# Optimization experiments

Measured on AMD Instinct MI355X. Metric: run time of the kernel, lower is better.

Reference implementation:

```python
import jax, jax.numpy as jnp
import numpy as np

PATCH = 16
CH = 3


def setup_inputs() -> dict:
    key = jax.random.key(0)
    k1, k2, k3 = jax.random.split(key, 3)
    B, H = 16, 512
    embed_dim = PATCH * PATCH * CH  # 768
    x = jax.random.normal(k1, (B, CH, H, H), dtype=jnp.float32)
    fan_in = CH * PATCH * PATCH
    w = jax.random.normal(k2, (embed_dim, CH, PATCH, PATCH), dtype=jnp.float32) / np.float32(np.sqrt(fan_in))
    b = jax.random.normal(k3, (embed_dim,), dtype=jnp.float32) * 0.01
    return {"x": x, "w": w, "b": b}


def reference(x, w, b):
    p = w.shape[2]                      # patch_size
    B, C, imgsize, _ = x.shape
    pn = imgsize // p                   # patch_num (NOTE: pre-padding count, as in source)
    # zero-pad by one patch on every side
    xp = jnp.pad(x, ((0, 0), (0, 0), (p, p), (p, p)))
    # strided patch-embed conv: [B, embed_dim, pn+2, pn+2]
    xt = jax.lax.conv_general_dilated(xp, w, window_strides=(p, p), padding='VALID')
    xt = xt + b[None, :, None, None]
    B1, C1, H1, W1 = xt.shape           # H1 = W1 = pn + 2
    xt = xt.reshape(B1, C1, H1 * W1)
    # same (buggy-looking but faithful) index set / stride-pn neighbors as the source
    idxs = jnp.array([i * pn + j for i in range(1, pn - 1) for j in range(1, pn)], dtype=jnp.int32)
    inv8 = jnp.float32(1.0 / 8.0)

    def body(buf, idx):
        # torch aliases x_final=x_temp, so reads see earlier in-place writes -> sequential scan
        s = (buf[:, :, idx - pn] + buf[:, :, idx + pn]
             + buf[:, :, idx - 1] + buf[:, :, idx + 1]
             + buf[:, :, idx - pn - 1] + buf[:, :, idx - pn + 1]
             + buf[:, :, idx + pn - 1] + buf[:, :, idx + pn + 1]) * inv8
        return buf.at[:, :, idx].set(s), None

    xf, _ = jax.lax.scan(body, xt, idxs)
    side = imgsize + 2 * p              # embed_dim*H1*W1 == C*side*side by construction
    out = xf.reshape(B1, C, side, side)
    return out[:, :, p:imgsize + p, p:imgsize + p]
```

## Files before the change

kernel.cpp:

```cpp
#include <hip/hip_runtime.h>
#include <hip/hip_bf16.h>


typedef __attribute__((ext_vector_type(8))) short s8v;
typedef __attribute__((ext_vector_type(4))) float f4v;
typedef __attribute__((ext_vector_type(8))) unsigned short us8;
typedef __attribute__((ext_vector_type(4))) unsigned short us4;

__device__ __forceinline__ unsigned short f2bf(float f) {
    __hip_bfloat16 h = __float2bfloat16(f);
    return *reinterpret_cast<unsigned short*>(&h);
}
__device__ __forceinline__ float bf2f(unsigned short u) {
    union { unsigned int i; float f; } c; c.i = (unsigned int)u << 16; return c.f;
}

__device__ __forceinline__ void gload_lds16(const void* g, void* l) {
    __builtin_amdgcn_global_load_lds(
        (const __attribute__((address_space(1))) unsigned int*)g,
        (__attribute__((address_space(3))) unsigned int*)l,
        16, 0, 0);
}

__global__ __launch_bounds__(256) void prep_k(const float* __restrict__ x,
                                              const float* __restrict__ w,
                                              unsigned short* __restrict__ a_bf,
                                              unsigned short* __restrict__ w_bf) {
    const int bid = blockIdx.x;
    if (bid < 6144) {
        int g = bid * 256 + threadIdx.x;
        int f = g << 3;
        int wc = f & 511;
        int h  = (f >> 9) & 511;
        int cb = f >> 18;
        int c  = cb % 3, b = cb / 3;
        const float4 v0 = *(const float4*)(x + f);
        const float4 v1 = *(const float4*)(x + f + 4);
        int m = (b << 10) + ((h >> 4) << 5) + (wc >> 4);
        int k = (c << 8) + ((h & 15) << 4) + (wc & 15);
        us8 o;
        o[0] = f2bf(v0.x); o[1] = f2bf(v0.y); o[2] = f2bf(v0.z); o[3] = f2bf(v0.w);
        o[4] = f2bf(v1.x); o[5] = f2bf(v1.y); o[6] = f2bf(v1.z); o[7] = f2bf(v1.w);
        *(us8*)(a_bf + (size_t)m * 768 + k) = o;
    } else {
        int g = (bid - 6144) * 256 + threadIdx.x;
        int f = g << 3;
        const float4 v0 = *(const float4*)(w + f);
        const float4 v1 = *(const float4*)(w + f + 4);
        us8 u;
        u[0] = f2bf(v0.x); u[1] = f2bf(v0.y); u[2] = f2bf(v0.z); u[3] = f2bf(v0.w);
        u[4] = f2bf(v1.x); u[5] = f2bf(v1.y); u[6] = f2bf(v1.z); u[7] = f2bf(v1.w);
        *(us8*)(w_bf + f) = u;
    }
}

__global__ __launch_bounds__(256) void conv_gemm_k(const unsigned short* __restrict__ A,
                                                   const unsigned short* __restrict__ W,
                                                   const float* __restrict__ bias,
                                                   unsigned short* __restrict__ xt) {
    __shared__ __align__(16) unsigned short As[2][128 * 32];
    __shared__ __align__(16) unsigned short Bs[2][128 * 32];
    const int tid  = threadIdx.x;
    const int lane = tid & 63, wv = tid >> 6;
    const int wr = wv >> 1, wc = wv & 1;
    const int m0 = blockIdx.x << 7, n0 = blockIdx.y << 7;
    const int bb = m0 >> 10;

    f4v acc[4][4] = {};

    const int l2 = lane >> 2;
    const int kx = ((lane & 3) ^ ((l2 >> 1) & 3)) << 3;
    const unsigned short* gA = A + (size_t)(m0 + (wv << 5) + l2) * 768 + kx;
    const unsigned short* gB = W + (size_t)(n0 + (wv << 5) + l2) * 768 + kx;

    auto stage = [&](int buf, int k0) {
        gload_lds16(gA + k0,            As[buf] + (wv << 10));
        gload_lds16(gA + k0 + 16 * 768, As[buf] + (wv << 10) + 512);
        gload_lds16(gB + k0,            Bs[buf] + (wv << 10));
        gload_lds16(gB + k0 + 16 * 768, Bs[buf] + (wv << 10) + 512);
    };

    stage(0, 0);
    asm volatile("s_waitcnt vmcnt(0)" ::: "memory");
    __syncthreads();

    const int cq = lane >> 4, l15 = lane & 15;
    int cur = 0;
    for (int t = 0; t < 24; ++t) {
        if (t < 23) stage(cur ^ 1, (t + 1) << 5);
        s8v a[4], b[4];
        #pragma unroll
        for (int mi = 0; mi < 4; ++mi) {
            int ra = (wr << 6) + (mi << 4) + l15;
            a[mi] = *(const s8v*)(As[cur] + (ra << 5) + ((cq ^ ((ra >> 1) & 3)) << 3));
        }
        #pragma unroll
        for (int ni = 0; ni < 4; ++ni) {
            int rb = (wc << 6) + (ni << 4) + l15;
            b[ni] = *(const s8v*)(Bs[cur] + (rb << 5) + ((cq ^ ((rb >> 1) & 3)) << 3));
        }
        #pragma unroll
        for (int mi = 0; mi < 4; ++mi)
            #pragma unroll
            for (int ni = 0; ni < 4; ++ni)
                acc[mi][ni] = __builtin_amdgcn_mfma_f32_16x16x32_bf16(a[mi], b[ni], acc[mi][ni], 0, 0, 0);
        asm volatile("s_waitcnt vmcnt(0)" ::: "memory");
        __syncthreads();
        cur ^= 1;
    }

    #pragma unroll
    for (int mi = 0; mi < 4; ++mi) {
        int m  = m0 + (wr << 6) + (mi << 4) + (cq << 2);
        int ph = (m >> 5) & 31, pwm = m & 31;
        unsigned short* dst = xt + (((size_t)bb * 768) << 10) + (ph << 5) + pwm;
        #pragma unroll
        for (int ni = 0; ni < 4; ++ni) {
            int n = n0 + (wc << 6) + (ni << 4) + l15;
            float bv = bias[n];
            us4 o;
            o[0] = f2bf(acc[mi][ni][0] + bv);
            o[1] = f2bf(acc[mi][ni][1] + bv);
            o[2] = f2bf(acc[mi][ni][2] + bv);
            o[3] = f2bf(acc[mi][ni][3] + bv);
            *(us4*)(dst + ((size_t)n << 10)) = o;
        }
    }
}

__global__ __launch_bounds__(256) void scan_emit_k(const unsigned short* __restrict__ xt,
                                                   const float* __restrict__ bias,
                                                   float* __restrict__ out) {
    const int grp = (blockIdx.x * 256 + threadIdx.x) >> 5;
    const int j   = threadIdx.x & 31;
    const int b   = grp / 768;
    const int c1  = grp - b * 768;
    const unsigned short* basep = xt + ((size_t)grp << 10);
    const float bias_c = bias[c1];
    float* baseo = out + (size_t)b * 786432 + (size_t)(c1 >> 8) * 262144;

    int rem = (c1 & 255) * 1156 + j;
    int ey  = rem / 544;
    int ex  = rem - ey * 544;
    int eo  = (ey - 16) * 512 + (ex - 16);

    auto estep = [&](float v) {
        if (((unsigned)(ex - 16) < 512u) & ((unsigned)(ey - 16) < 512u))
            baseo[eo] = v;
        ex += 32;
        int wrp = (ex >= 544);
        ex -= wrp ? 544 : 0;
        ey += wrp;
        eo += wrp ? 0 : 32;
    };
    auto sel = [&](int p) -> float {
        unsigned int h = (unsigned int)p / 34u;
        unsigned int w = (unsigned int)p - h * 34u;
        if ((h == 0u) | (h == 33u) | (w == 0u) | (w == 33u)) return bias_c;
        return bf2f(basep[(h - 1u) * 32u + (w - 1u)]);
    };

    float co = sel( 32 + j);
    float no = sel( 64 + j);
    float o2 = sel( 96 + j);
    float o3 = sel(128 + j);
    estep(bias_c);
    float pn   = bias_c;
    float po_h = bias_c;
    float h_co = __shfl(co, 0, 32);
    float h_no = __shfl(no, 0, 32);
    float h_o2 = __shfl(o2, 0, 32);
    float rr   = __shfl_down(co, 1, 32);
    if (j == 31) rr = h_no;

    for (int i = 1; i <= 30; ++i) {
        float ld = sel((i + 4) * 32 + j);
        float UL = __shfl_up(pn, 1, 32);   if (j == 1)  UL = po_h;
        float UR = __shfl_down(pn, 1, 32); if (j == 31) UR = h_co;
        float D1 = __shfl_up(no, 1, 32);
        float D3 = __shfl_down(no, 1, 32); if (j == 31) D3 = h_o2;
        float bv = (((UL + pn) + (UR + rr)) + ((D1 + no) + D3)) * 0.125f;
        if (j == 1) bv += h_co * 0.125f;
        float t;
        t = __shfl_up(bv, 1, 32);  bv += (j > 1) ? 0.125f * t : 0.f;
        t = __shfl_up(bv, 2, 32);  bv += (j > 2) ? 0.015625f * t : 0.f;
        t = __shfl_up(bv, 4, 32);  bv += (j > 4) ? 2.44140625e-4f * t : 0.f;
        estep((j == 0) ? co : bv);
        rr   = D3;
        pn   = bv;
        po_h = h_co; h_co = h_no; h_no = h_o2;
        h_o2 = __shfl(o3, 0, 32);
        co = no; no = o2; o2 = o3; o3 = ld;
    }
    estep(co);
    estep(no);
    estep(o2);
    estep(o3);
    estep(sel(1120 + j));
    if (j < 4) estep(bias_c);
}

extern "C" void kernel_launch(void* const* d_in, const int* in_sizes, int n_in,
                              void* d_out, int out_size, void* d_ws, size_t ws_size,
                              hipStream_t stream) {
    const float* x    = (const float*)d_in[0];
    const float* w    = (const float*)d_in[1];
    const float* bias = (const float*)d_in[2];
    float* out = (float*)d_out;
    unsigned short* xt = (unsigned short*)d_ws;

    unsigned short* a_bf = (unsigned short*)d_out;
    unsigned short* w_bf = a_bf + (size_t)16384 * 768;

    prep_k<<<6432, 256, 0, stream>>>(x, w, a_bf, w_bf);
    conv_gemm_k<<<dim3(128, 6), 256, 0, stream>>>(a_bf, w_bf, bias, xt);
    scan_emit_k<<<1536, 256, 0, stream>>>(xt, bias, out);
}
```

Before: 78.68 us.

## Fuse im2col and bf16 conversion of x into the conv GEMM A-tile loads

Removes the separate pass that converted x to bf16 in patch-major layout. The GEMM now loads fp32 image rows straight into LDS with global_load_lds and converts them to bf16 while reading A fragments. The prefetch pipeline also becomes two tiles deep, with split barriers and partial vmcnt waits. This saves a full read and write of the 50 MB activation buffer, at the cost of twice the LDS for A, more VALU conversion work per MFMA, and fp32 A tiles being re-read by all 6 N-blocks.

New measurement: 76.17 us. 1.03x faster.

```diff
diff --git a/kernel.cpp b/kernel.cpp
--- a/kernel.cpp
+++ b/kernel.cpp
@@ -22,91 +22,95 @@
         16, 0, 0);
 }
 
-__global__ __launch_bounds__(256) void prep_k(const float* __restrict__ x,
-                                              const float* __restrict__ w,
-                                              unsigned short* __restrict__ a_bf,
-                                              unsigned short* __restrict__ w_bf) {
-    const int bid = blockIdx.x;
-    if (bid < 6144) {
-        int g = bid * 256 + threadIdx.x;
-        int f = g << 3;
-        int wc = f & 511;
-        int h  = (f >> 9) & 511;
-        int cb = f >> 18;
-        int c  = cb % 3, b = cb / 3;
-        const float4 v0 = *(const float4*)(x + f);
-        const float4 v1 = *(const float4*)(x + f + 4);
-        int m = (b << 10) + ((h >> 4) << 5) + (wc >> 4);
-        int k = (c << 8) + ((h & 15) << 4) + (wc & 15);
-        us8 o;
-        o[0] = f2bf(v0.x); o[1] = f2bf(v0.y); o[2] = f2bf(v0.z); o[3] = f2bf(v0.w);
-        o[4] = f2bf(v1.x); o[5] = f2bf(v1.y); o[6] = f2bf(v1.z); o[7] = f2bf(v1.w);
-        *(us8*)(a_bf + (size_t)m * 768 + k) = o;
-    } else {
-        int g = (bid - 6144) * 256 + threadIdx.x;
-        int f = g << 3;
-        const float4 v0 = *(const float4*)(w + f);
-        const float4 v1 = *(const float4*)(w + f + 4);
-        us8 u;
-        u[0] = f2bf(v0.x); u[1] = f2bf(v0.y); u[2] = f2bf(v0.z); u[3] = f2bf(v0.w);
-        u[4] = f2bf(v1.x); u[5] = f2bf(v1.y); u[6] = f2bf(v1.z); u[7] = f2bf(v1.w);
-        *(us8*)(w_bf + f) = u;
-    }
-}
-
-__global__ __launch_bounds__(256) void conv_gemm_k(const unsigned short* __restrict__ A,
+__global__ __launch_bounds__(256) void prep_w_k(const float* __restrict__ w,
+                                                unsigned short* __restrict__ w_bf) {
+    int g = blockIdx.x * 256 + threadIdx.x;
+    int f = g << 3;
+    const float4 v0 = *(const float4*)(w + f);
+    const float4 v1 = *(const float4*)(w + f + 4);
+    us8 u;
+    u[0] = f2bf(v0.x); u[1] = f2bf(v0.y); u[2] = f2bf(v0.z); u[3] = f2bf(v0.w);
+    u[4] = f2bf(v1.x); u[5] = f2bf(v1.y); u[6] = f2bf(v1.z); u[7] = f2bf(v1.w);
+    *(us8*)(w_bf + f) = u;
+}
+
+__global__ __launch_bounds__(256) void conv_gemm_k(const float* __restrict__ x,
                                                    const unsigned short* __restrict__ W,
                                                    const float* __restrict__ bias,
                                                    unsigned short* __restrict__ xt) {
-    __shared__ __align__(16) unsigned short As[2][128 * 32];
+    __shared__ __align__(16) float          Asf[2][128 * 32];
     __shared__ __align__(16) unsigned short Bs[2][128 * 32];
     const int tid  = threadIdx.x;
     const int lane = tid & 63, wv = tid >> 6;
     const int wr = wv >> 1, wc = wv & 1;
     const int m0 = blockIdx.x << 7, n0 = blockIdx.y << 7;
     const int bb = m0 >> 10;
+    const int ph0 = (m0 >> 5) & 31;
 
     f4v acc[4][4] = {};
+
+    const int clog = (lane & 7) ^ ((lane >> 3) & 7);
+    const float* abase = x + (size_t)bb * 786432
+                           + ((ph0 + wv) * 16 + (clog >> 2)) * 512 + ((clog & 3) << 2);
+    const float* asrc[4];
+    #pragma unroll
+    for (int i = 0; i < 4; ++i) asrc[i] = abase + ((i * 8 + (lane >> 3)) << 4);
 
     const int l2 = lane >> 2;
     const int kx = ((lane & 3) ^ ((l2 >> 1) & 3)) << 3;
-    const unsigned short* gA = A + (size_t)(m0 + (wv << 5) + l2) * 768 + kx;
     const unsigned short* gB = W + (size_t)(n0 + (wv << 5) + l2) * 768 + kx;
 
-    auto stage = [&](int buf, int k0) {
-        gload_lds16(gA + k0,            As[buf] + (wv << 10));
-        gload_lds16(gA + k0 + 16 * 768, As[buf] + (wv << 10) + 512);
+    auto stage = [&](int buf, int t) {
+        const int koff = (t >> 3) * 262144 + (t & 7) * 1024;
+        #pragma unroll
+        for (int i = 0; i < 4; ++i)
+            gload_lds16(asrc[i] + koff, Asf[buf] + (wv << 10) + (i << 8));
+        const int k0 = t << 5;
         gload_lds16(gB + k0,            Bs[buf] + (wv << 10));
         gload_lds16(gB + k0 + 16 * 768, Bs[buf] + (wv << 10) + 512);
     };
 
     stage(0, 0);
-    asm volatile("s_waitcnt vmcnt(0)" ::: "memory");
-    __syncthreads();
+    stage(1, 1);
+    asm volatile("s_waitcnt vmcnt(6)" ::: "memory");
+    asm volatile("s_barrier" ::: "memory");
 
     const int cq = lane >> 4, l15 = lane & 15;
-    int cur = 0;
     for (int t = 0; t < 24; ++t) {
-        if (t < 23) stage(cur ^ 1, (t + 1) << 5);
+        const int p = t & 1;
         s8v a[4], b[4];
         #pragma unroll
         for (int mi = 0; mi < 4; ++mi) {
-            int ra = (wr << 6) + (mi << 4) + l15;
-            a[mi] = *(const s8v*)(As[cur] + (ra << 5) + ((cq ^ ((ra >> 1) & 3)) << 3));
+            int r    = (wr << 6) + (mi << 4) + l15;
+            int base = ((r >> 5) << 10) + ((r & 31) << 5);
+            int s    = r & 7;
+            float4 f0 = *(const float4*)(Asf[p] + base + ((((cq << 1))     ^ s) << 2));
+            float4 f1 = *(const float4*)(Asf[p] + base + ((((cq << 1) | 1) ^ s) << 2));
+            s8v av;
+            av[0] = (short)f2bf(f0.x); av[1] = (short)f2bf(f0.y);
+            av[2] = (short)f2bf(f0.z); av[3] = (short)f2bf(f0.w);
+            av[4] = (short)f2bf(f1.x); av[5] = (short)f2bf(f1.y);
+            av[6] = (short)f2bf(f1.z); av[7] = (short)f2bf(f1.w);
+            a[mi] = av;
         }
         #pragma unroll
         for (int ni = 0; ni < 4; ++ni) {
             int rb = (wc << 6) + (ni << 4) + l15;
-            b[ni] = *(const s8v*)(Bs[cur] + (rb << 5) + ((cq ^ ((rb >> 1) & 3)) << 3));
+            b[ni] = *(const s8v*)(Bs[p] + (rb << 5) + ((cq ^ ((rb >> 1) & 3)) << 3));
         }
         #pragma unroll
         for (int mi = 0; mi < 4; ++mi)
             #pragma unroll
             for (int ni = 0; ni < 4; ++ni)
                 acc[mi][ni] = __builtin_amdgcn_mfma_f32_16x16x32_bf16(a[mi], b[ni], acc[mi][ni], 0, 0, 0);
-        asm volatile("s_waitcnt vmcnt(0)" ::: "memory");
-        __syncthreads();
-        cur ^= 1;
+        asm volatile("s_barrier" ::: "memory");
+        if (t < 22) {
+            stage(p, t + 2);
+            asm volatile("s_waitcnt vmcnt(6)" ::: "memory");
+        } else {
+            asm volatile("s_waitcnt vmcnt(0)" ::: "memory");
+        }
+        asm volatile("s_barrier" ::: "memory");
     }
 
     #pragma unroll
@@ -209,10 +213,9 @@
     float* out = (float*)d_out;
     unsigned short* xt = (unsigned short*)d_ws;
 
-    unsigned short* a_bf = (unsigned short*)d_out;
-    unsigned short* w_bf = a_bf + (size_t)16384 * 768;
-
-    prep_k<<<6432, 256, 0, stream>>>(x, w, a_bf, w_bf);
-    conv_gemm_k<<<dim3(128, 6), 256, 0, stream>>>(a_bf, w_bf, bias, xt);
+    unsigned short* w_bf = (unsigned short*)d_out;
+
+    prep_w_k<<<288, 256, 0, stream>>>(w, w_bf);
+    conv_gemm_k<<<dim3(128, 6), 256, 0, stream>>>(x, w_bf, bias, xt);
     scan_emit_k<<<1536, 256, 0, stream>>>(xt, bias, out);
 }
```
